# Kernel optimization log

Measured on AMD Instinct MI355X. Metric: run time of the kernel, lower is better.

Reference implementation:

```python
import jax, jax.numpy as jnp
import numpy as np

BS = 4096
FD = 768   # feature_dim
PD = 500   # proj_dim
ZD = 300   # z_dim
R = 10     # retrieval_num
U = 10     # retrieval_user_num
N_PER = 3 + 2 * R + U  # 33 nodes per sample


def _lin(x, w, b):
    return x @ w.T + b


def _build_incidence(bs, r, u):
    # Faithful to get_hyper_edge_index_and_weight: 4 group edges per sample
    # plus R pair edges that (as in the original code) omit the batch bias,
    # i.e. always reference sample-0 nodes. dhg.Hypergraph dedups duplicate
    # edges, so the R pair edges appear once.
    n = 3 + 2 * r + u
    node_list, edge_list = [], []
    e = 0
    for b in range(bs):
        o = b * n
        groups = [
            list(range(o, o + 3)),
            list(range(o + 3, o + 3 + r)) + [o],
            list(range(o + 3 + r, o + 3 + 2 * r)) + [o + 1],
            list(range(o + 3 + 2 * r, o + n)) + [o + 2],
        ]
        for g in groups:
            node_list.extend(g)
            edge_list.extend([e] * len(g))
            e += 1
    for i in range(r):
        node_list.extend([3 + i, 3 + r + i])
        edge_list.extend([e, e])
        e += 1
    return np.asarray(node_list, np.int32), np.asarray(edge_list, np.int32), e


def setup_inputs() -> dict:
    key = jax.random.key(0)
    ks = jax.random.split(key, 32)

    def rn(k, shape, s=1.0):
        return jax.random.normal(k, shape, dtype=jnp.float32) * s

    inp = {
        "visual_feature": rn(ks[0], (BS, 1, FD)),
        "textual_feature": rn(ks[1], (BS, 1, FD)),
        "similarity": rn(ks[2], (BS, R)),
        "retrieved_visual_feature": rn(ks[3], (BS, R, 1, FD)),
        "retrieved_textual_feature": rn(ks[4], (BS, R, FD)),
        "retrieved_label": jax.random.uniform(ks[5], (BS, R, 1), dtype=jnp.float32),
        "user": rn(ks[6], (BS, FD)),
        "retrieved_user": rn(ks[7], (BS, U, FD)),
        "retrieved_user_similarity": rn(ks[8], (BS, U)),
        # learned params (0.02-scaled normal init)
        "vis_w": rn(ks[9], (PD, FD), 0.02), "vis_b": jnp.zeros((PD,), jnp.float32),
        "txt_w": rn(ks[10], (PD, FD), 0.02), "txt_b": jnp.zeros((PD,), jnp.float32),
        "usr_w": rn(ks[11], (PD, FD), 0.02), "usr_b": jnp.zeros((PD,), jnp.float32),
        "rvis_w": rn(ks[12], (PD, FD), 0.02), "rvis_b": jnp.zeros((PD,), jnp.float32),
        "rtxt_w": rn(ks[13], (PD, FD), 0.02), "rtxt_b": jnp.zeros((PD,), jnp.float32),
        "rusr_w": rn(ks[14], (PD, FD), 0.02), "rusr_b": jnp.zeros((PD,), jnp.float32),
        "hg_w": rn(ks[15], (ZD, PD), 0.02), "hg_b": jnp.zeros((ZD,), jnp.float32),
        "lbl_w": rn(ks[16], (ZD, 1), 0.02), "lbl_b": jnp.zeros((ZD,), jnp.float32),
        "p1_w": rn(ks[17], (800, ZD * 7), 0.02), "p1_b": jnp.zeros((800,), jnp.float32),
        "p2_w": rn(ks[18], (200, 800), 0.02), "p2_b": jnp.zeros((200,), jnp.float32),
        "p3_w": rn(ks[19], (1, 200), 0.02), "p3_b": jnp.zeros((1,), jnp.float32),
    }
    return inp


def reference(visual_feature, textual_feature, similarity, retrieved_visual_feature,
              retrieved_textual_feature, retrieved_label, user, retrieved_user,
              retrieved_user_similarity,
              vis_w, vis_b, txt_w, txt_b, usr_w, usr_b,
              rvis_w, rvis_b, rtxt_w, rtxt_b, rusr_w, rusr_b,
              hg_w, hg_b, lbl_w, lbl_b,
              p1_w, p1_b, p2_w, p2_b, p3_w, p3_b):
    bs = visual_feature.shape[0]
    # dense tanh embeddings -> per-sample node feature block [bs, 33, 500]
    t = jnp.tanh(_lin(textual_feature, txt_w, txt_b))
    v = jnp.tanh(_lin(visual_feature, vis_w, vis_b))
    u = jnp.tanh(_lin(user[:, None, :], usr_w, usr_b))
    rt = jnp.tanh(_lin(retrieved_textual_feature, rtxt_w, rtxt_b))
    rv = jnp.tanh(_lin(retrieved_visual_feature[:, :, 0, :], rvis_w, rvis_b))
    ru = jnp.tanh(_lin(retrieved_user, rusr_w, rusr_b))
    X = jnp.concatenate([t, v, u, rt, rv, ru], axis=1).reshape(-1, PD)  # [bs*33, 500]

    # hypergraph conv (HGNN+ layer, softmax_then_sum over unit incidence == mean)
    node_ids, edge_ids, E = _build_incidence(bs, R, U)  # static, built at trace time
    N = X.shape[0]
    Xt = _lin(X, hg_w, hg_b)  # theta: [N, 300]
    ones = jnp.ones(node_ids.shape[0], jnp.float32)
    deg_e = jax.ops.segment_sum(ones, edge_ids, num_segments=E)
    Y = jax.ops.segment_sum(Xt[node_ids], edge_ids, num_segments=E) / deg_e[:, None]
    deg_v = jax.ops.segment_sum(ones, node_ids, num_segments=N)
    Xo = jax.ops.segment_sum(Y[edge_ids], node_ids, num_segments=N) / deg_v[:, None]
    Xo = jax.nn.relu(Xo).reshape(bs, N_PER, ZD)

    # retrieval aggregation: softmax-weighted sums over retrieved sets
    sim = jax.nn.softmax(similarity, axis=1)                      # [bs, R]
    usim = jax.nn.softmax(retrieved_user_similarity, axis=1)      # [bs, U]
    rt_agg = jnp.einsum('br,brd->bd', sim, Xo[:, 3:3 + R, :])
    rv_agg = jnp.einsum('br,brd->bd', sim, Xo[:, 3 + R:3 + 2 * R, :])
    ru_agg = jnp.einsum('br,brd->bd', usim, Xo[:, 3 + 2 * R:3 + 2 * R + U, :])
    lbl_agg = jnp.einsum('br,bro->bo', sim, retrieved_label)      # [bs, 1]
    lbl_emb = jax.nn.relu(_lin(lbl_agg, lbl_w, lbl_b))            # [bs, 300]

    feat = jnp.concatenate(
        [Xo[:, 0, :], Xo[:, 1, :], Xo[:, 2, :], rv_agg, rt_agg, ru_agg, lbl_emb], axis=1)
    h = jax.nn.relu(_lin(feat, p1_w, p1_b))
    h = jax.nn.relu(_lin(h, p2_w, p2_b))
    out = jax.nn.sigmoid(_lin(h, p3_w, p3_b))  # [bs, 1]
    return out
```

## Files before the change

kernel.cpp:

```cpp
#include <hip/hip_runtime.h>
#include <math.h>

#define BS 4096
#define FD 768
#define PD 500
#define ZD 300
#define RNUM 10
#define SD 512

typedef short bf16x8 __attribute__((ext_vector_type(8)));
typedef float f32x4 __attribute__((ext_vector_type(4)));

__device__ __forceinline__ unsigned int fbits(float f) {
  union { float f; unsigned int u; } v; v.f = f; return v.u;
}

__device__ __forceinline__ unsigned int pack2bf(float f0, float f1) {
  unsigned int u0 = fbits(f0) + 0x8000u;
  unsigned int u1 = fbits(f1) + 0x8000u;
  return __builtin_amdgcn_perm(u1, u0, 0x07060302u);
}

#define BM 128
#define BN 64
#define BK 16
#define TM 8
#define TN 4
template <int ACT>
__global__ __launch_bounds__(256) void gemm_kernel(
    const float* __restrict__ A, const float* __restrict__ W,
    const float* __restrict__ bias, float* __restrict__ C,
    int M, int N, int K) {
  __shared__ float As[BK][BM + 4];
  __shared__ float Bs[BK][BN + 4];
  const int m0 = blockIdx.x * BM;
  const int n0 = blockIdx.y * BN;
  const int tid = threadIdx.x;
  const int tx = tid & 15;
  const int ty = tid >> 4;
  float acc[TM][TN];
#pragma unroll
  for (int i = 0; i < TM; i++)
#pragma unroll
    for (int j = 0; j < TN; j++) acc[i][j] = 0.f;
  const int l_row = tid >> 2;
  const int l_k4 = (tid & 3) * 4;
  for (int k0 = 0; k0 < K; k0 += BK) {
#pragma unroll
    for (int half = 0; half < 2; ++half) {
      int m = m0 + l_row + half * 64;
      int k = k0 + l_k4;
      float4 v = make_float4(0.f, 0.f, 0.f, 0.f);
      if (m < M && k + 4 <= K) v = *(const float4*)(A + (size_t)m * K + k);
      As[l_k4 + 0][l_row + half * 64] = v.x;
      As[l_k4 + 1][l_row + half * 64] = v.y;
      As[l_k4 + 2][l_row + half * 64] = v.z;
      As[l_k4 + 3][l_row + half * 64] = v.w;
    }
    {
      int n = n0 + l_row;
      int k = k0 + l_k4;
      float4 v = make_float4(0.f, 0.f, 0.f, 0.f);
      if (n < N && k + 4 <= K) v = *(const float4*)(W + (size_t)n * K + k);
      Bs[l_k4 + 0][l_row] = v.x;
      Bs[l_k4 + 1][l_row] = v.y;
      Bs[l_k4 + 2][l_row] = v.z;
      Bs[l_k4 + 3][l_row] = v.w;
    }
    __syncthreads();
#pragma unroll
    for (int k = 0; k < BK; k++) {
      float a[TM], b[TN];
#pragma unroll
      for (int i = 0; i < TM; i++) a[i] = As[k][ty * TM + i];
#pragma unroll
      for (int j = 0; j < TN; j++) b[j] = Bs[k][tx * TN + j];
#pragma unroll
      for (int i = 0; i < TM; i++)
#pragma unroll
        for (int j = 0; j < TN; j++) acc[i][j] += a[i] * b[j];
    }
    __syncthreads();
  }
#pragma unroll
  for (int i = 0; i < TM; i++) {
    int m = m0 + ty * TM + i;
    if (m >= M) continue;
#pragma unroll
    for (int j = 0; j < TN; j++) {
      int n = n0 + tx * TN + j;
      if (n >= N) continue;
      float v = acc[i][j] + bias[n];
      if (ACT == 1) v = fmaxf(v, 0.f);
      C[(size_t)m * N + n] = v;
    }
  }
}

__global__ __launch_bounds__(256) void padcast_tileB(
    const float* __restrict__ src, unsigned short* __restrict__ dst,
    int rs, int cs, int rowsPerTile, int nRowTiles, int NT) {
  const int total = nRowTiles * NT * rowsPerTile * 4;
  int i = blockIdx.x * 256 + threadIdx.x;
  if (i >= total) return;
  const int gpt = rowsPerTile * 4;
  int nb = i / (NT * gpt);
  int rem1 = i - nb * NT * gpt;
  int t = rem1 / gpt;
  int rem = rem1 - t * gpt;
  int row = rem >> 2;
  int slot = rem & 3;
  int gq = slot ^ ((row >> 1) & 3);
  int grow = nb * rowsPerTile + row;
  float f[8];
#pragma unroll
  for (int e = 0; e < 8; e++) {
    int k = t * 32 + gq * 8 + e;
    f[e] = (grow < rs && k < cs) ? src[(size_t)grow * cs + k] : 0.f;
  }
  uint4 o;
  o.x = pack2bf(f[0], f[1]);
  o.y = pack2bf(f[2], f[3]);
  o.z = pack2bf(f[4], f[5]);
  o.w = pack2bf(f[6], f[7]);
  *(uint4*)(dst + (size_t)i * 8) = o;
}

template <int ACT>
__global__ __launch_bounds__(256) void mfma_gemm(
    const float* __restrict__ A, int lda, int Ka,
    const unsigned short* __restrict__ B, int NT,
    const float* __restrict__ bias, float* __restrict__ C, int Nout) {
  __shared__ unsigned short ldsA[2][128 * 32];
  __shared__ unsigned short ldsB[2][128 * 32];
  const int tid = threadIdx.x;
  const int n0 = blockIdx.x * 128;
  const int m0 = blockIdx.y * 128;

  const int arow = tid >> 1;
  const int ahalf = (tid & 1) << 4;
  const int ag = (tid & 1) << 1;
  const int aswz = (arow >> 1) & 3;
  const int aw0 = (arow * 4 + ((ag | 0) ^ aswz)) * 8;
  const int aw1 = (arow * 4 + ((ag | 1) ^ aswz)) * 8;
  const float* aptr = A + (size_t)(m0 + arow) * lda;
  const unsigned short* bbase = B + (size_t)blockIdx.x * NT * 4096 + (size_t)tid * 8;

  const int lane = tid & 63;
  const int wave = tid >> 6;
  const int wm = (wave >> 1) << 6;
  const int wn = (wave & 1) << 6;
  const int r16 = lane & 15;
  const int kq = lane >> 4;

  int afoff[4], bfoff[4];
#pragma unroll
  for (int i = 0; i < 4; i++) {
    int rowA = wm + i * 16 + r16;
    afoff[i] = (rowA * 4 + (kq ^ ((rowA >> 1) & 3))) * 8;
    int rowB = wn + i * 16 + r16;
    bfoff[i] = (rowB * 4 + (kq ^ ((rowB >> 1) & 3))) * 8;
  }

  f32x4 acc[4][4] = {};

  float4 f[4];
  uint4 bv0, bv1;
#pragma unroll
  for (int q = 0; q < 4; q++) {
    int k = ahalf + q * 4;
    f[q] = (k < Ka) ? *(const float4*)(aptr + k) : make_float4(0.f, 0.f, 0.f, 0.f);
  }
  bv0 = *(const uint4*)(bbase + 0);
  bv1 = *(const uint4*)(bbase + 2048);
  {
    uint4 w0, w1;
    w0.x = pack2bf(f[0].x, f[0].y); w0.y = pack2bf(f[0].z, f[0].w);
    w0.z = pack2bf(f[1].x, f[1].y); w0.w = pack2bf(f[1].z, f[1].w);
    w1.x = pack2bf(f[2].x, f[2].y); w1.y = pack2bf(f[2].z, f[2].w);
    w1.z = pack2bf(f[3].x, f[3].y); w1.w = pack2bf(f[3].z, f[3].w);
    *(uint4*)&ldsA[0][aw0] = w0;
    *(uint4*)&ldsA[0][aw1] = w1;
    *(uint4*)&ldsB[0][tid * 8] = bv0;
    *(uint4*)&ldsB[0][tid * 8 + 2048] = bv1;
  }

#pragma unroll 2
  for (int t = 0; t < NT; ++t) {
    const int cb = t & 1;
    asm volatile("s_waitcnt lgkmcnt(0)" ::: "memory");
    __builtin_amdgcn_s_barrier();
    if (t + 1 < NT) {
      const int k0 = (t + 1) << 5;
#pragma unroll
      for (int q = 0; q < 4; q++) {
        int k = k0 + ahalf + q * 4;
        f[q] = (k < Ka) ? *(const float4*)(aptr + k)
                        : make_float4(0.f, 0.f, 0.f, 0.f);
      }
      bv0 = *(const uint4*)(bbase + (size_t)(t + 1) * 4096);
      bv1 = *(const uint4*)(bbase + (size_t)(t + 1) * 4096 + 2048);
    }
    bf16x8 a[4], b[4];
#pragma unroll
    for (int i = 0; i < 4; i++) a[i] = *(const bf16x8*)&ldsA[cb][afoff[i]];
#pragma unroll
    for (int i = 0; i < 4; i++) b[i] = *(const bf16x8*)&ldsB[cb][bfoff[i]];
#pragma unroll
    for (int i = 0; i < 4; i++)
#pragma unroll
      for (int j = 0; j < 4; j++)
        acc[i][j] = __builtin_amdgcn_mfma_f32_16x16x32_bf16(a[i], b[j], acc[i][j], 0, 0, 0);
    if (t + 1 < NT) {
      uint4 w0, w1;
      w0.x = pack2bf(f[0].x, f[0].y); w0.y = pack2bf(f[0].z, f[0].w);
      w0.z = pack2bf(f[1].x, f[1].y); w0.w = pack2bf(f[1].z, f[1].w);
      w1.x = pack2bf(f[2].x, f[2].y); w1.y = pack2bf(f[2].z, f[2].w);
      w1.z = pack2bf(f[3].x, f[3].y); w1.w = pack2bf(f[3].z, f[3].w);
      *(uint4*)&ldsA[cb ^ 1][aw0] = w0;
      *(uint4*)&ldsA[cb ^ 1][aw1] = w1;
      *(uint4*)&ldsB[cb ^ 1][tid * 8] = bv0;
      *(uint4*)&ldsB[cb ^ 1][tid * 8 + 2048] = bv1;
    }
  }

#pragma unroll
  for (int j = 0; j < 4; j++) {
    int n = n0 + wn + j * 16 + r16;
    if (n >= Nout) continue;
    float bi = bias[n];
#pragma unroll
    for (int i = 0; i < 4; i++) {
#pragma unroll
      for (int r = 0; r < 4; r++) {
        int m = m0 + wm + i * 16 + kq * 4 + r;
        float v = acc[i][j][r] + bi;
        if (ACT == 1) v = fmaxf(v, 0.f);
        C[(size_t)m * Nout + n] = v;
      }
    }
  }
}

struct EmbedArgs {
  const float* A[6];
  const float* bias[6];
};

__global__ __launch_bounds__(512, 2) void embed_mfma(
    EmbedArgs ea, const unsigned short* __restrict__ Wbf,
    float* __restrict__ S, float* __restrict__ E0) {
  __shared__ unsigned short ldsA[2][128 * 32];
  __shared__ unsigned short ldsB[2][512 * 32];
  const int tid = threadIdx.x;
  const int m0 = blockIdx.x * 128;

  int g, base;
  if (m0 < 4096) { g = 0; base = 0; }
  else if (m0 < 8192) { g = 1; base = 4096; }
  else if (m0 < 12288) { g = 2; base = 8192; }
  else if (m0 < 53248) { g = 3; base = 12288; }
  else if (m0 < 94208) { g = 4; base = 53248; }
  else { g = 5; base = 94208; }

  const int arow = tid >> 2;
  const int aq = tid & 3;
  const int aswz = (arow >> 1) & 3;
  const int awoff = (arow * 4 + (aq ^ aswz)) * 8;
  const float* aptr = ea.A[g] + (size_t)(m0 - base + arow) * FD + aq * 8;

  const unsigned short* bbase = Wbf + (size_t)g * (24 * 16384) + (size_t)tid * 8;

  const int lane = tid & 63;
  const int wave = tid >> 6;
  const int wm = (wave >> 2) << 6;
  const int wn = (wave & 3) << 7;
  const int r16 = lane & 15;
  const int kq = lane >> 4;

  int afoff[4], bfoff[8];
#pragma unroll
  for (int i = 0; i < 4; i++) {
    int rowA = wm + i * 16 + r16;
    afoff[i] = (rowA * 4 + (kq ^ ((rowA >> 1) & 3))) * 8;
  }
#pragma unroll
  for (int j = 0; j < 8; j++) {
    int rowB = wn + j * 16 + r16;
    bfoff[j] = (rowB * 4 + (kq ^ ((rowB >> 1) & 3))) * 8;
  }

  f32x4 acc[4][8] = {};

  float4 fa0 = *(const float4*)(aptr + 0);
  float4 fa1 = *(const float4*)(aptr + 4);
  uint4 bv[4];
#pragma unroll
  for (int q = 0; q < 4; q++) bv[q] = *(const uint4*)(bbase + q * 4096);
  {
    uint4 aw;
    aw.x = pack2bf(fa0.x, fa0.y); aw.y = pack2bf(fa0.z, fa0.w);
    aw.z = pack2bf(fa1.x, fa1.y); aw.w = pack2bf(fa1.z, fa1.w);
    *(uint4*)&ldsA[0][awoff] = aw;
#pragma unroll
    for (int q = 0; q < 4; q++) *(uint4*)&ldsB[0][tid * 8 + q * 4096] = bv[q];
  }

  const int NT = FD / 32;
#pragma unroll 2
  for (int t = 0; t < NT; ++t) {
    const int cb = t & 1;
    asm volatile("s_waitcnt lgkmcnt(0)" ::: "memory");
    __builtin_amdgcn_s_barrier();
    if (t + 1 < NT) {
      const float* ap = aptr + (t + 1) * 32;
      fa0 = *(const float4*)(ap + 0);
      fa1 = *(const float4*)(ap + 4);
      const unsigned short* bp = bbase + (size_t)(t + 1) * 16384;
#pragma unroll
      for (int q = 0; q < 4; q++) bv[q] = *(const uint4*)(bp + q * 4096);
    }
    bf16x8 a[4], b[8];
#pragma unroll
    for (int i = 0; i < 4; i++) a[i] = *(const bf16x8*)&ldsA[cb][afoff[i]];
#pragma unroll
    for (int j = 0; j < 8; j++) b[j] = *(const bf16x8*)&ldsB[cb][bfoff[j]];
#pragma unroll
    for (int i = 0; i < 4; i++)
#pragma unroll
      for (int j = 0; j < 8; j++)
        acc[i][j] = __builtin_amdgcn_mfma_f32_16x16x32_bf16(a[i], b[j], acc[i][j], 0, 0, 0);
    if (t + 1 < NT) {
      uint4 aw;
      aw.x = pack2bf(fa0.x, fa0.y); aw.y = pack2bf(fa0.z, fa0.w);
      aw.z = pack2bf(fa1.x, fa1.y); aw.w = pack2bf(fa1.z, fa1.w);
      *(uint4*)&ldsA[cb ^ 1][awoff] = aw;
#pragma unroll
      for (int q = 0; q < 4; q++)
        *(uint4*)&ldsB[cb ^ 1][tid * 8 + q * 4096] = bv[q];
    }
  }

  const float* bias = ea.bias[g];
  if (g < 3) {
#pragma unroll
    for (int j = 0; j < 8; j++) {
      int n = wn + j * 16 + r16;
      if (n >= PD) continue;
      float bi = bias[n];
#pragma unroll
      for (int i = 0; i < 4; i++) {
#pragma unroll
        for (int r = 0; r < 4; r++) {
          int rl = m0 - base + wm + i * 16 + kq * 4 + r;
          S[((size_t)g * BS + rl) * SD + n] = tanhf(acc[i][j][r] + bi);
        }
      }
    }
    return;
  }

  const int R0 = m0 - base;
  const int b0 = R0 / 10;
  const int b1 = (R0 + 127) / 10;
  const int ng = b1 - b0 + 1;
  float* red = (float*)&ldsB[0][0];
  const int myc = wave & 3;
  __syncthreads();
#pragma unroll
  for (int ch = 0; ch < 8; ++ch) {
    if ((ch >> 1) == myc) {
#pragma unroll
      for (int jj = 0; jj < 4; jj++) {
        int j = ((ch & 1) << 2) + jj;
        int n = wn + j * 16 + r16;
        int cl = (jj << 4) + r16;
        float bi = (n < PD) ? bias[n] : 0.f;
#pragma unroll
        for (int i = 0; i < 4; i++) {
#pragma unroll
          for (int r = 0; r < 4; r++) {
            int row = wm + i * 16 + kq * 4 + r;
            red[row * 68 + cl] = acc[i][j][r] + bi;
          }
        }
      }
    }
    __syncthreads();
    for (int task = tid; task < ng * 64; task += 512) {
      int cl = task & 63;
      int bb = b0 + (task >> 6);
      int n = (ch << 6) + cl;
      if (n < PD) {
        int rlo = bb * 10 - R0;
        int rhi = rlo + 9;
        int lo = rlo < 0 ? 0 : rlo;
        int hi = rhi > 127 ? 127 : rhi;
        float s = 0.f;
        for (int r = lo; r <= hi; r++) s += tanhf(red[r * 68 + cl]);
        size_t idx = ((size_t)g * BS + bb) * SD + n;
        if (hi - lo == 9) S[idx] = s;
        else atomicAdd(&S[idx], s);
        if (g != 5 && bb == 0 && R0 == 0) {
#pragma unroll
          for (int rr = 0; rr < 10; rr++)
            E0[((size_t)(g - 3) * 10 + rr) * PD + n] = tanhf(red[rr * 68 + cl]);
        }
      }
    }
    __syncthreads();
  }
}

__global__ __launch_bounds__(256) void means_kernel(
    const float* __restrict__ S, float* __restrict__ Mn) {
  const int total = 4 * BS * PD;
  const size_t P = (size_t)BS * SD;
  for (int i = blockIdx.x * blockDim.x + threadIdx.x; i < total;
       i += gridDim.x * blockDim.x) {
    int m = i / PD;
    int k = i - m * PD;
    int b = m >> 2, e = m & 3;
    float v;
    const size_t o = (size_t)b * SD + k;
    if (e == 0)
      v = (S[o] + S[P + o] + S[2 * P + o]) * (1.f / 3.f);
    else if (e == 1)
      v = (S[3 * P + o] + S[o]) * (1.f / 11.f);
    else if (e == 2)
      v = (S[4 * P + o] + S[P + o]) * (1.f / 11.f);
    else
      v = (S[5 * P + o] + S[2 * P + o]) * (1.f / 11.f);
    Mn[i] = v;
  }
}

__global__ __launch_bounds__(256) void xte_kernel(
    const float* __restrict__ E0, const float* __restrict__ hg_w,
    const float* __restrict__ hg_b, float* __restrict__ XtE) {
  const int i = blockIdx.x;
  __shared__ float row[PD];
  for (int k = threadIdx.x; k < PD; k += 256) row[k] = E0[(size_t)i * PD + k];
  __syncthreads();
  for (int n = threadIdx.x; n < ZD; n += 256) {
    float s = 0.f;
    const float* w = hg_w + (size_t)n * PD;
    for (int k = 0; k < PD; k++) s += row[k] * w[k];
    XtE[(size_t)i * ZD + n] = s + hg_b[n];
  }
}

__global__ __launch_bounds__(256) void feat_kernel(
    const float* __restrict__ Y, const float* __restrict__ XtE,
    const float* __restrict__ sim_in, const float* __restrict__ label,
    const float* __restrict__ lbl_w, const float* __restrict__ lbl_b,
    float* __restrict__ feat) {
  const int b = blockIdx.x;
  __shared__ float w[RNUM];
  __shared__ float lbl_agg_s;
  if (threadIdx.x == 0) {
    float s[RNUM], mx = -1e30f;
    for (int r = 0; r < RNUM; r++) {
      s[r] = sim_in[(size_t)b * RNUM + r];
      mx = fmaxf(mx, s[r]);
    }
    float sum = 0.f;
    for (int r = 0; r < RNUM; r++) { s[r] = expf(s[r] - mx); sum += s[r]; }
    float la = 0.f;
    for (int r = 0; r < RNUM; r++) {
      w[r] = s[r] / sum;
      la += w[r] * label[(size_t)b * RNUM + r];
    }
    lbl_agg_s = la;
  }
  __syncthreads();
  const float* Yb = Y + (size_t)b * 4 * ZD;
  float* fb = feat + (size_t)b * 7 * ZD;
  const float la = lbl_agg_s;
  for (int n = threadIdx.x; n < ZD; n += blockDim.x) {
    float y0 = Yb[n], y1 = Yb[ZD + n], y2 = Yb[2 * ZD + n], y3 = Yb[3 * ZD + n];
    fb[n] = fmaxf(0.5f * (y0 + y1), 0.f);
    fb[ZD + n] = fmaxf(0.5f * (y0 + y2), 0.f);
    fb[2 * ZD + n] = fmaxf(0.5f * (y0 + y3), 0.f);
    float rv, rt;
    if (b == 0) {
      rv = 0.f; rt = 0.f;
      for (int r = 0; r < RNUM; r++) {
        float yp = 0.5f * (XtE[(size_t)r * ZD + n] + XtE[(size_t)(10 + r) * ZD + n]);
        rt += w[r] * fmaxf(0.5f * (y1 + yp), 0.f);
        rv += w[r] * fmaxf(0.5f * (y2 + yp), 0.f);
      }
    } else {
      rt = fmaxf(y1, 0.f);
      rv = fmaxf(y2, 0.f);
    }
    fb[3 * ZD + n] = rv;
    fb[4 * ZD + n] = rt;
    fb[5 * ZD + n] = fmaxf(y3, 0.f);
    fb[6 * ZD + n] = fmaxf(la * lbl_w[n] + lbl_b[n], 0.f);
  }
}

__global__ __launch_bounds__(256) void head_kernel(
    const float* __restrict__ h2, const float* __restrict__ p3_w,
    const float* __restrict__ p3_b, float* __restrict__ out) {
  const int wave = (blockIdx.x * blockDim.x + threadIdx.x) >> 6;
  const int lane = threadIdx.x & 63;
  if (wave >= BS) return;
  const float* row = h2 + (size_t)wave * 200;
  float s = 0.f;
  for (int k = lane; k < 200; k += 64) s += row[k] * p3_w[k];
#pragma unroll
  for (int off = 32; off; off >>= 1) s += __shfl_down(s, off, 64);
  if (lane == 0) out[wave] = 1.f / (1.f + expf(-(s + p3_b[0])));
}

extern "C" void kernel_launch(void* const* d_in, const int* in_sizes, int n_in,
                              void* d_out, int out_size, void* d_ws,
                              size_t ws_size, hipStream_t stream) {
  (void)in_sizes; (void)n_in; (void)out_size; (void)ws_size;

  const float* visual = (const float*)d_in[0];
  const float* textual = (const float*)d_in[1];
  const float* similarity = (const float*)d_in[2];
  const float* r_visual = (const float*)d_in[3];
  const float* r_textual = (const float*)d_in[4];
  const float* r_label = (const float*)d_in[5];
  const float* user = (const float*)d_in[6];
  const float* r_user = (const float*)d_in[7];
  const float* vis_w = (const float*)d_in[9];
  const float* vis_b = (const float*)d_in[10];
  const float* txt_w = (const float*)d_in[11];
  const float* txt_b = (const float*)d_in[12];
  const float* usr_w = (const float*)d_in[13];
  const float* usr_b = (const float*)d_in[14];
  const float* rvis_w = (const float*)d_in[15];
  const float* rvis_b = (const float*)d_in[16];
  const float* rtxt_w = (const float*)d_in[17];
  const float* rtxt_b = (const float*)d_in[18];
  const float* rusr_w = (const float*)d_in[19];
  const float* rusr_b = (const float*)d_in[20];
  const float* hg_w = (const float*)d_in[21];
  const float* hg_b = (const float*)d_in[22];
  const float* lbl_w = (const float*)d_in[23];
  const float* lbl_b = (const float*)d_in[24];
  const float* p1_w = (const float*)d_in[25];
  const float* p1_b = (const float*)d_in[26];
  const float* p2_w = (const float*)d_in[27];
  const float* p2_b = (const float*)d_in[28];
  const float* p3_w = (const float*)d_in[29];
  const float* p3_b = (const float*)d_in[30];
  float* out = (float*)d_out;

  float* ws = (float*)d_ws;
  float* S = ws;
  float* E0 = S + (size_t)6 * BS * SD;
  float* XtE = E0 + 20 * PD;
  float* Mn = XtE + 20 * ZD;
  float* Y = Mn + (size_t)4 * BS * PD;
  float* feat = Y + (size_t)4 * BS * ZD;
  float* h1 = feat + (size_t)BS * 7 * ZD;
  float* h2 = h1 + (size_t)BS * 800;
  unsigned short* Wbf = (unsigned short*)(h2 + (size_t)BS * 200);
  unsigned short* hgwbf = Wbf + (size_t)6 * 24 * 16384;
  unsigned short* p1wbf = hgwbf + (size_t)3 * 16 * 4096;

  const float* ew[6] = {txt_w, vis_w, usr_w, rtxt_w, rvis_w, rusr_w};
  for (int g = 0; g < 6; g++) {
    padcast_tileB<<<(24 * 512 * 4 + 255) / 256, 256, 0, stream>>>(
        ew[g], Wbf + (size_t)g * 24 * 16384, PD, FD, 512, 1, 24);
  }
  padcast_tileB<<<(3 * 16 * 128 * 4 + 255) / 256, 256, 0, stream>>>(
      hg_w, hgwbf, ZD, PD, 128, 3, 16);
  padcast_tileB<<<(7 * 66 * 128 * 4 + 255) / 256, 256, 0, stream>>>(
      p1_w, p1wbf, 800, 2100, 128, 7, 66);

  hipMemsetAsync(S + (size_t)3 * BS * SD, 0, (size_t)3 * BS * SD * sizeof(float),
                 stream);

  EmbedArgs ea;
  ea.A[0] = textual;  ea.bias[0] = txt_b;
  ea.A[1] = visual;   ea.bias[1] = vis_b;
  ea.A[2] = user;     ea.bias[2] = usr_b;
  ea.A[3] = r_textual; ea.bias[3] = rtxt_b;
  ea.A[4] = r_visual;  ea.bias[4] = rvis_b;
  ea.A[5] = r_user;    ea.bias[5] = rusr_b;

  embed_mfma<<<dim3(135168 / 128), 512, 0, stream>>>(ea, Wbf, S, E0);
  xte_kernel<<<20, 256, 0, stream>>>(E0, hg_w, hg_b, XtE);
  means_kernel<<<4096, 256, 0, stream>>>(S, Mn);
  mfma_gemm<0><<<dim3(3, 16384 / 128), 256, 0, stream>>>(
      Mn, PD, PD, hgwbf, 16, hg_b, Y, ZD);
  feat_kernel<<<BS, 256, 0, stream>>>(Y, XtE, similarity, r_label, lbl_w, lbl_b,
                                      feat);
  mfma_gemm<1><<<dim3(7, BS / 128), 256, 0, stream>>>(
      feat, 2100, 2100, p1wbf, 66, p1_b, h1, 800);
  gemm_kernel<1><<<dim3(BS / BM, (200 + BN - 1) / BN), 256, 0, stream>>>(
      h1, p2_w, p2_b, h2, BS, 200, 800);
  head_kernel<<<BS * 64 / 256, 256, 0, stream>>>(h2, p3_w, p3_b, out);
}
```

Before: 1.075 ms.

## Load B fragments directly from global into registers, dropping LDS staging for weights

The pre-tiled bf16 weight matrix is now stored unswizzled, and each lane loads its MFMA B fragments straight from global memory into double-buffered registers. This removes the B tiles from LDS in both the generic GEMM and the embedding GEMM, so only A goes through LDS. The main loops are manually unrolled by two with register ping-pong. The smaller LDS footprint allows higher occupancy hints in launch bounds. The cost is redundant global/L2 traffic for B across waves that share columns, plus higher register pressure.

```diff
diff --git a/kernel.cpp b/kernel.cpp
--- a/kernel.cpp
+++ b/kernel.cpp
@@ -109,8 +109,7 @@
   int t = rem1 / gpt;
   int rem = rem1 - t * gpt;
   int row = rem >> 2;
-  int slot = rem & 3;
-  int gq = slot ^ ((row >> 1) & 3);
+  int gq = rem & 3;
   int grow = nb * rowsPerTile + row;
   float f[8];
 #pragma unroll
@@ -126,13 +125,47 @@
   *(uint4*)(dst + (size_t)i * 8) = o;
 }
 
+#define GM_STEP(T, CUROFF, NXTOFF, BCUR, BNXT)                               \
+  {                                                                          \
+    asm volatile("s_waitcnt lgkmcnt(0)" ::: "memory");                       \
+    __builtin_amdgcn_s_barrier();                                            \
+    const bool pf = (T) + 1 < NT;                                            \
+    float4 f[4];                                                             \
+    if (pf) {                                                                \
+      const int k0 = ((T) + 1) << 5;                                         \
+      _Pragma("unroll") for (int q = 0; q < 4; q++) {                        \
+        int k = k0 + ahalf + q * 4;                                          \
+        f[q] = (k < Ka) ? *(const float4*)(aptr + k)                         \
+                        : make_float4(0.f, 0.f, 0.f, 0.f);                   \
+      }                                                                      \
+      const unsigned short* bp = bg + (size_t)((T) + 1) * 4096;              \
+      _Pragma("unroll") for (int j = 0; j < 4; j++)                          \
+          BNXT[j] = *(const uint4*)(bp + j * 512);                           \
+    }                                                                        \
+    bf16x8 a[4];                                                             \
+    _Pragma("unroll") for (int i = 0; i < 4; i++)                            \
+        a[i] = *(const bf16x8*)&ldsA[(CUROFF) + afoff[i]];                   \
+    _Pragma("unroll") for (int i = 0; i < 4; i++)                            \
+      _Pragma("unroll") for (int j = 0; j < 4; j++)                          \
+        acc[i][j] = __builtin_amdgcn_mfma_f32_16x16x32_bf16(                 \
+            a[i], *(const bf16x8*)&BCUR[j], acc[i][j], 0, 0, 0);             \
+    if (pf) {                                                                \
+      uint4 w0, w1;                                                          \
+      w0.x = pack2bf(f[0].x, f[0].y); w0.y = pack2bf(f[0].z, f[0].w);        \
+      w0.z = pack2bf(f[1].x, f[1].y); w0.w = pack2bf(f[1].z, f[1].w);        \
+      w1.x = pack2bf(f[2].x, f[2].y); w1.y = pack2bf(f[2].z, f[2].w);        \
+      w1.z = pack2bf(f[3].x, f[3].y); w1.w = pack2bf(f[3].z, f[3].w);        \
+      *(uint4*)&ldsA[(NXTOFF) + aw0] = w0;                                   \
+      *(uint4*)&ldsA[(NXTOFF) + aw1] = w1;                                   \
+    }                                                                        \
+  }
+
 template <int ACT>
-__global__ __launch_bounds__(256) void mfma_gemm(
+__global__ __launch_bounds__(256, 8) void mfma_gemm(
     const float* __restrict__ A, int lda, int Ka,
     const unsigned short* __restrict__ B, int NT,
     const float* __restrict__ bias, float* __restrict__ C, int Nout) {
-  __shared__ unsigned short ldsA[2][128 * 32];
-  __shared__ unsigned short ldsB[2][128 * 32];
+  __shared__ unsigned short ldsA[2 * 128 * 32];
   const int tid = threadIdx.x;
   const int n0 = blockIdx.x * 128;
   const int m0 = blockIdx.y * 128;
@@ -144,7 +177,6 @@
   const int aw0 = (arow * 4 + ((ag | 0) ^ aswz)) * 8;
   const int aw1 = (arow * 4 + ((ag | 1) ^ aswz)) * 8;
   const float* aptr = A + (size_t)(m0 + arow) * lda;
-  const unsigned short* bbase = B + (size_t)blockIdx.x * NT * 4096 + (size_t)tid * 8;
 
   const int lane = tid & 63;
   const int wave = tid >> 6;
@@ -153,75 +185,40 @@
   const int r16 = lane & 15;
   const int kq = lane >> 4;
 
-  int afoff[4], bfoff[4];
+  int afoff[4];
 #pragma unroll
   for (int i = 0; i < 4; i++) {
     int rowA = wm + i * 16 + r16;
     afoff[i] = (rowA * 4 + (kq ^ ((rowA >> 1) & 3))) * 8;
-    int rowB = wn + i * 16 + r16;
-    bfoff[i] = (rowB * 4 + (kq ^ ((rowB >> 1) & 3))) * 8;
-  }
+  }
+  const unsigned short* bg =
+      B + (size_t)blockIdx.x * NT * 4096 + ((size_t)(wn + r16) * 4 + kq) * 8;
 
   f32x4 acc[4][4] = {};
-
-  float4 f[4];
-  uint4 bv0, bv1;
-#pragma unroll
-  for (int q = 0; q < 4; q++) {
-    int k = ahalf + q * 4;
-    f[q] = (k < Ka) ? *(const float4*)(aptr + k) : make_float4(0.f, 0.f, 0.f, 0.f);
-  }
-  bv0 = *(const uint4*)(bbase + 0);
-  bv1 = *(const uint4*)(bbase + 2048);
+  uint4 bA4[4], bB4[4];
+
+#pragma unroll
+  for (int j = 0; j < 4; j++) bA4[j] = *(const uint4*)(bg + j * 512);
   {
+    float4 f[4];
+#pragma unroll
+    for (int q = 0; q < 4; q++) {
+      int k = ahalf + q * 4;
+      f[q] = (k < Ka) ? *(const float4*)(aptr + k)
+                      : make_float4(0.f, 0.f, 0.f, 0.f);
+    }
     uint4 w0, w1;
     w0.x = pack2bf(f[0].x, f[0].y); w0.y = pack2bf(f[0].z, f[0].w);
     w0.z = pack2bf(f[1].x, f[1].y); w0.w = pack2bf(f[1].z, f[1].w);
     w1.x = pack2bf(f[2].x, f[2].y); w1.y = pack2bf(f[2].z, f[2].w);
     w1.z = pack2bf(f[3].x, f[3].y); w1.w = pack2bf(f[3].z, f[3].w);
-    *(uint4*)&ldsA[0][aw0] = w0;
-    *(uint4*)&ldsA[0][aw1] = w1;
-    *(uint4*)&ldsB[0][tid * 8] = bv0;
-    *(uint4*)&ldsB[0][tid * 8 + 2048] = bv1;
-  }
-
-#pragma unroll 2
-  for (int t = 0; t < NT; ++t) {
-    const int cb = t & 1;
-    asm volatile("s_waitcnt lgkmcnt(0)" ::: "memory");
-    __builtin_amdgcn_s_barrier();
-    if (t + 1 < NT) {
-      const int k0 = (t + 1) << 5;
-#pragma unroll
-      for (int q = 0; q < 4; q++) {
-        int k = k0 + ahalf + q * 4;
-        f[q] = (k < Ka) ? *(const float4*)(aptr + k)
-                        : make_float4(0.f, 0.f, 0.f, 0.f);
-      }
-      bv0 = *(const uint4*)(bbase + (size_t)(t + 1) * 4096);
-      bv1 = *(const uint4*)(bbase + (size_t)(t + 1) * 4096 + 2048);
-    }
-    bf16x8 a[4], b[4];
-#pragma unroll
-    for (int i = 0; i < 4; i++) a[i] = *(const bf16x8*)&ldsA[cb][afoff[i]];
-#pragma unroll
-    for (int i = 0; i < 4; i++) b[i] = *(const bf16x8*)&ldsB[cb][bfoff[i]];
-#pragma unroll
-    for (int i = 0; i < 4; i++)
-#pragma unroll
-      for (int j = 0; j < 4; j++)
-        acc[i][j] = __builtin_amdgcn_mfma_f32_16x16x32_bf16(a[i], b[j], acc[i][j], 0, 0, 0);
-    if (t + 1 < NT) {
-      uint4 w0, w1;
-      w0.x = pack2bf(f[0].x, f[0].y); w0.y = pack2bf(f[0].z, f[0].w);
-      w0.z = pack2bf(f[1].x, f[1].y); w0.w = pack2bf(f[1].z, f[1].w);
-      w1.x = pack2bf(f[2].x, f[2].y); w1.y = pack2bf(f[2].z, f[2].w);
-      w1.z = pack2bf(f[3].x, f[3].y); w1.w = pack2bf(f[3].z, f[3].w);
-      *(uint4*)&ldsA[cb ^ 1][aw0] = w0;
-      *(uint4*)&ldsA[cb ^ 1][aw1] = w1;
-      *(uint4*)&ldsB[cb ^ 1][tid * 8] = bv0;
-      *(uint4*)&ldsB[cb ^ 1][tid * 8 + 2048] = bv1;
-    }
+    *(uint4*)&ldsA[aw0] = w0;
+    *(uint4*)&ldsA[aw1] = w1;
+  }
+
+  for (int tt = 0; tt < NT; tt += 2) {
+    GM_STEP(tt, 0, 4096, bA4, bB4);
+    GM_STEP(tt + 1, 4096, 0, bB4, bA4);
   }
 
 #pragma unroll
@@ -247,11 +244,40 @@
   const float* bias[6];
 };
 
-__global__ __launch_bounds__(512, 2) void embed_mfma(
+#define EMB_STEP(T, CUROFF, NXTOFF, BCUR, BNXT)                              \
+  {                                                                          \
+    asm volatile("s_waitcnt lgkmcnt(0)" ::: "memory");                       \
+    __builtin_amdgcn_s_barrier();                                            \
+    const bool pf = (T) + 1 < NT;                                            \
+    float4 fa0, fa1;                                                         \
+    if (pf) {                                                                \
+      const float* ap = aptr + ((T) + 1) * 32;                               \
+      fa0 = *(const float4*)(ap);                                            \
+      fa1 = *(const float4*)(ap + 4);                                        \
+      const unsigned short* bp = bg + (size_t)((T) + 1) * 16384;             \
+      _Pragma("unroll") for (int j = 0; j < 8; j++)                          \
+          BNXT[j] = *(const uint4*)(bp + j * 512);                           \
+    }                                                                        \
+    bf16x8 a[4];                                                             \
+    _Pragma("unroll") for (int i = 0; i < 4; i++)                            \
+        a[i] = *(const bf16x8*)&ldsA[(CUROFF) + afoff[i]];                   \
+    _Pragma("unroll") for (int i = 0; i < 4; i++)                            \
+      _Pragma("unroll") for (int j = 0; j < 8; j++)                          \
+        acc[i][j] = __builtin_amdgcn_mfma_f32_16x16x32_bf16(                 \
+            a[i], *(const bf16x8*)&BCUR[j], acc[i][j], 0, 0, 0);             \
+    if (pf) {                                                                \
+      uint4 aw;                                                              \
+      aw.x = pack2bf(fa0.x, fa0.y); aw.y = pack2bf(fa0.z, fa0.w);            \
+      aw.z = pack2bf(fa1.x, fa1.y); aw.w = pack2bf(fa1.z, fa1.w);            \
+      *(uint4*)&ldsA[(NXTOFF) + awoff] = aw;                                 \
+    }                                                                        \
+  }
+
+__global__ __launch_bounds__(512, 6) void embed_mfma(
     EmbedArgs ea, const unsigned short* __restrict__ Wbf,
     float* __restrict__ S, float* __restrict__ E0) {
-  __shared__ unsigned short ldsA[2][128 * 32];
-  __shared__ unsigned short ldsB[2][512 * 32];
+  __shared__ __align__(16) unsigned char smem[34816];
+  unsigned short* ldsA = (unsigned short*)smem;
   const int tid = threadIdx.x;
   const int m0 = blockIdx.x * 128;
 
@@ -269,8 +295,6 @@
   const int awoff = (arow * 4 + (aq ^ aswz)) * 8;
   const float* aptr = ea.A[g] + (size_t)(m0 - base + arow) * FD + aq * 8;
 
-  const unsigned short* bbase = Wbf + (size_t)g * (24 * 16384) + (size_t)tid * 8;
-
   const int lane = tid & 63;
   const int wave = tid >> 6;
   const int wm = (wave >> 2) << 6;
@@ -278,67 +302,33 @@
   const int r16 = lane & 15;
   const int kq = lane >> 4;
 
-  int afoff[4], bfoff[8];
+  int afoff[4];
 #pragma unroll
   for (int i = 0; i < 4; i++) {
     int rowA = wm + i * 16 + r16;
     afoff[i] = (rowA * 4 + (kq ^ ((rowA >> 1) & 3))) * 8;
   }
-#pragma unroll
-  for (int j = 0; j < 8; j++) {
-    int rowB = wn + j * 16 + r16;
-    bfoff[j] = (rowB * 4 + (kq ^ ((rowB >> 1) & 3))) * 8;
-  }
+  const unsigned short* bg =
+      Wbf + (size_t)g * (24 * 16384) + ((size_t)(wn + r16) * 4 + kq) * 8;
 
   f32x4 acc[4][8] = {};
-
-  float4 fa0 = *(const float4*)(aptr + 0);
-  float4 fa1 = *(const float4*)(aptr + 4);
-  uint4 bv[4];
-#pragma unroll
-  for (int q = 0; q < 4; q++) bv[q] = *(const uint4*)(bbase + q * 4096);
+  uint4 bA[8], bB[8];
+  const int NT = FD / 32;
+
+#pragma unroll
+  for (int j = 0; j < 8; j++) bA[j] = *(const uint4*)(bg + j * 512);
   {
+    float4 fa0 = *(const float4*)(aptr);
+    float4 fa1 = *(const float4*)(aptr + 4);
     uint4 aw;
     aw.x = pack2bf(fa0.x, fa0.y); aw.y = pack2bf(fa0.z, fa0.w);
     aw.z = pack2bf(fa1.x, fa1.y); aw.w = pack2bf(fa1.z, fa1.w);
-    *(uint4*)&ldsA[0][awoff] = aw;
-#pragma unroll
-    for (int q = 0; q < 4; q++) *(uint4*)&ldsB[0][tid * 8 + q * 4096] = bv[q];
-  }
-
-  const int NT = FD / 32;
-#pragma unroll 2
-  for (int t = 0; t < NT; ++t) {
-    const int cb = t & 1;
-    asm volatile("s_waitcnt lgkmcnt(0)" ::: "memory");
-    __builtin_amdgcn_s_barrier();
-    if (t + 1 < NT) {
-      const float* ap = aptr + (t + 1) * 32;
-      fa0 = *(const float4*)(ap + 0);
-      fa1 = *(const float4*)(ap + 4);
-      const unsigned short* bp = bbase + (size_t)(t + 1) * 16384;
-#pragma unroll
-      for (int q = 0; q < 4; q++) bv[q] = *(const uint4*)(bp + q * 4096);
-    }
-    bf16x8 a[4], b[8];
-#pragma unroll
-    for (int i = 0; i < 4; i++) a[i] = *(const bf16x8*)&ldsA[cb][afoff[i]];
-#pragma unroll
-    for (int j = 0; j < 8; j++) b[j] = *(const bf16x8*)&ldsB[cb][bfoff[j]];
-#pragma unroll
-    for (int i = 0; i < 4; i++)
-#pragma unroll
-      for (int j = 0; j < 8; j++)
-        acc[i][j] = __builtin_amdgcn_mfma_f32_16x16x32_bf16(a[i], b[j], acc[i][j], 0, 0, 0);
-    if (t + 1 < NT) {
-      uint4 aw;
-      aw.x = pack2bf(fa0.x, fa0.y); aw.y = pack2bf(fa0.z, fa0.w);
-      aw.z = pack2bf(fa1.x, fa1.y); aw.w = pack2bf(fa1.z, fa1.w);
-      *(uint4*)&ldsA[cb ^ 1][awoff] = aw;
-#pragma unroll
-      for (int q = 0; q < 4; q++)
-        *(uint4*)&ldsB[cb ^ 1][tid * 8 + q * 4096] = bv[q];
-    }
+    *(uint4*)&ldsA[awoff] = aw;
+  }
+
+  for (int tt = 0; tt < NT; tt += 2) {
+    EMB_STEP(tt, 0, 4096, bA, bB);
+    EMB_STEP(tt + 1, 4096, 0, bB, bA);
   }
 
   const float* bias = ea.bias[g];
@@ -364,7 +354,7 @@
   const int b0 = R0 / 10;
   const int b1 = (R0 + 127) / 10;
   const int ng = b1 - b0 + 1;
-  float* red = (float*)&ldsB[0][0];
+  float* red = (float*)smem;
   const int myc = wave & 3;
   __syncthreads();
 #pragma unroll
```

New measurement: 4.263 ms. 297% more time.
